# Performance work log

Hardware: AMD Instinct MI355X
Metric: run time of the kernel (lower is better)

## Reference

```python
import jax, jax.numpy as jnp
import numpy as np

D_IN, D_OUT, ORDER, N = 1024, 8192, 3, 2048


def _make_hmap(key, d_in, d_out):
    k1, k2 = jax.random.split(key)
    # h = floor(rand * D_out), row index per input feature
    h = jnp.floor(jax.random.uniform(k1, (d_in,)) * d_out).astype(jnp.int32)
    # w = round(rand) * 2 - 1  -> +/-1 signs
    w = jnp.round(jax.random.uniform(k2, (d_in,))) * 2.0 - 1.0
    # dense [D_out, D_in] with exactly one nonzero per column (faithful to to_dense())
    hm = jnp.zeros((d_out, d_in), dtype=jnp.float32)
    return hm.at[h, jnp.arange(d_in)].set(w.astype(jnp.float32))


def setup_inputs() -> dict:
    key = jax.random.key(0)
    kx, kh = jax.random.split(key)
    x = jax.random.normal(kx, (D_IN, N), dtype=jnp.float32)
    hkeys = jax.random.split(kh, ORDER)
    hmaps = jnp.stack([_make_hmap(hkeys[i], D_IN, D_OUT) for i in range(ORDER)])  # [order, D_out, D_in]
    return {"x": x, "hmaps": hmaps}


def reference(x, hmaps):
    # count[i] = (hmaps[i] @ x).T : [order, N, D_out]
    count = jnp.einsum('odi,in->ond', hmaps, x)
    # torch.rfft(onesided=False) == full complex FFT along last dim
    F = jnp.fft.fft(count, axis=-1)  # complex64, [order, N, D_out]
    # P starts at 1+0j and accumulates complex products over orders
    P = jnp.prod(F, axis=0)  # [N, D_out]
    # torch.irfft(onesided=False) returns real part of inverse FFT
    result = jnp.fft.ifft(P, axis=-1).real.astype(x.dtype)  # [N, D_out]
    return result.T  # [D_out, N]
```

## Files before the change

### kernel.cpp

```cpp
#include <hip/hip_runtime.h>

#define D_IN   1024
#define D_OUTD 8192
#define ORDER  3
#define NCOL   2048

__device__ float2 g_tw[D_OUTD / 2];
__device__ int    g_h[ORDER * D_IN];
__device__ float  g_w[ORDER * D_IN];

__global__ void tw_kernel() {
    int k = blockIdx.x * 256 + threadIdx.x;
    if (k < D_OUTD / 2) {
        double ang = -2.0 * 3.14159265358979323846 * (double)k / (double)D_OUTD;
        g_tw[k] = make_float2((float)cos(ang), (float)sin(ang));
    }
}

__global__ void extract_kernel(const float* __restrict__ hmaps) {
    int idx = blockIdx.x * 256 + threadIdx.x;
    if (idx >= ORDER * D_OUTD * D_IN) return;
    float v = hmaps[idx];
    if (v != 0.0f) {
        int i   = idx % D_IN;
        int rem = idx / D_IN;
        int d   = rem % D_OUTD;
        int o   = rem / D_OUTD;
        g_h[o * D_IN + i] = d;
        g_w[o * D_IN + i] = v;
    }
}

__global__ void xt_kernel(const float* __restrict__ in, float* __restrict__ out) {
    __shared__ float tile[32][33];
    int i0 = blockIdx.x * 32;
    int n0 = blockIdx.y * 32;
    int tx = threadIdx.x;
    int ty = threadIdx.y;
#pragma unroll
    for (int j = 0; j < 32; j += 8)
        tile[ty + j][tx] = in[(i0 + ty + j) * NCOL + n0 + tx];
    __syncthreads();
#pragma unroll
    for (int j = 0; j < 32; j += 8)
        out[(n0 + ty + j) * D_IN + i0 + tx] = tile[tx][ty + j];
}

__device__ __forceinline__ float2 cmul(float2 a, float2 b) {
    return make_float2(a.x * b.x - a.y * b.y, a.x * b.y + a.y * b.x);
}
__device__ __forceinline__ float2 csqr(float2 a) {
    return make_float2(a.x * a.x - a.y * a.y, 2.0f * a.x * a.y);
}
__device__ __forceinline__ float2 c16(int k) {
    constexpr float R[8] = { 1.0f,  0.92387953251128674f,  0.70710678118654757f,  0.38268343236508978f,
                             0.0f, -0.38268343236508978f, -0.70710678118654757f, -0.92387953251128674f };
    constexpr float I[8] = { 0.0f, -0.38268343236508978f, -0.70710678118654757f, -0.92387953251128674f,
                            -1.0f, -0.92387953251128674f, -0.70710678118654757f, -0.38268343236508978f };
    return make_float2(R[k], I[k]);
}

#define FWD_FFT(XR, XI)                                                          \
    {                                                                            \
        float2 ba = wt;                                                          \
        _Pragma("unroll")                                                        \
        for (int m = 3; m >= 0; --m) {                                           \
            const int half = 1 << m;                                             \
            float2 tw[8];                                                        \
            _Pragma("unroll")                                                    \
            for (int lo = 0; lo < half; ++lo) tw[lo] = cmul(ba, c16(lo << (3 - m))); \
            _Pragma("unroll")                                                    \
            for (int p = 0; p < 8; ++p) {                                        \
                const int lo = p & (half - 1);                                   \
                const int hi = p >> m;                                           \
                const int j0 = (hi << (m + 1)) + lo;                             \
                const int j1 = j0 + half;                                        \
                const float2 w = tw[lo];                                         \
                float ar = XR[j0], ai = XI[j0];                                  \
                float br = XR[j1], bi = XI[j1];                                  \
                XR[j0] = ar + br; XI[j0] = ai + bi;                              \
                float dr = ar - br, di = ai - bi;                                \
                XR[j1] = dr * w.x - di * w.y;                                    \
                XI[j1] = dr * w.y + di * w.x;                                    \
            }                                                                    \
            if (m) ba = csqr(ba);                                                \
        }                                                                        \
    }                                                                            \
    _Pragma("unroll")                                                            \
    for (int j = 0; j < 16; ++j) { bre[t + 512 * j] = XR[j]; bim[t + 512 * j] = XI[j]; } \
    __syncthreads();                                                             \
    _Pragma("unroll")                                                            \
    for (int j = 0; j < 16; ++j) { XR[j] = bre[base + 32 * j]; XI[j] = bim[base + 32 * j]; } \
    __syncthreads();                                                             \
    {                                                                            \
        float2 bb = bb16;                                                        \
        _Pragma("unroll")                                                        \
        for (int m = 3; m >= 0; --m) {                                           \
            const int half = 1 << m;                                             \
            float2 tw[8];                                                        \
            _Pragma("unroll")                                                    \
            for (int lo = 0; lo < half; ++lo) tw[lo] = cmul(bb, c16(lo << (3 - m))); \
            _Pragma("unroll")                                                    \
            for (int p = 0; p < 8; ++p) {                                        \
                const int lo = p & (half - 1);                                   \
                const int hi = p >> m;                                           \
                const int j0 = (hi << (m + 1)) + lo;                             \
                const int j1 = j0 + half;                                        \
                const float2 w = tw[lo];                                         \
                float ar = XR[j0], ai = XI[j0];                                  \
                float br = XR[j1], bi = XI[j1];                                  \
                XR[j0] = ar + br; XI[j0] = ai + bi;                              \
                float dr = ar - br, di = ai - bi;                                \
                XR[j1] = dr * w.x - di * w.y;                                    \
                XI[j1] = dr * w.y + di * w.x;                                    \
            }                                                                    \
            if (m) bb = csqr(bb);                                                \
        }                                                                        \
    }                                                                            \
    _Pragma("unroll")                                                            \
    for (int lh = 4; lh >= 0; --lh) {                                            \
        const int st = 1 << lh;                                                  \
        float2 w = tc[lh];                                                       \
        const bool up = (s & st) != 0;                                           \
        const float sg = up ? -1.0f : 1.0f;                                      \
        if (!up) { w.x = 1.0f; w.y = 0.0f; }                                     \
        _Pragma("unroll")                                                        \
        for (int j = 0; j < 16; ++j) {                                           \
            float pr = __shfl_xor(XR[j], st, 64);                                \
            float pi = __shfl_xor(XI[j], st, 64);                                \
            float tr = pr + sg * XR[j];                                          \
            float ti = pi + sg * XI[j];                                          \
            XR[j] = tr * w.x - ti * w.y;                                         \
            XI[j] = tr * w.y + ti * w.x;                                         \
        }                                                                        \
    }

__launch_bounds__(512, 2)
__global__ void sketch_kernel(const float* __restrict__ x, float* __restrict__ outbuf,
                              int staged, int xcoal) {
    __shared__ float bre[D_OUTD];
    __shared__ float bim[D_OUTD];
    const int n0 = 2 * blockIdx.x;
    const int n1 = n0 + 1;
    const int t = threadIdx.x;
    const int s = t & 31;
    const int base = ((t >> 5) << 9) + s;

    float xA0, xA1, xB0, xB1;
    if (xcoal) {
        xA0 = x[n0 * D_IN + t]; xA1 = x[n0 * D_IN + t + 512];
        xB0 = x[n1 * D_IN + t]; xB1 = x[n1 * D_IN + t + 512];
    } else {
        xA0 = x[t * NCOL + n0]; xA1 = x[(t + 512) * NCOL + n0];
        xB0 = x[t * NCOL + n1]; xB1 = x[(t + 512) * NCOL + n1];
    }

    const float2 wt  = g_tw[t];
    const float2 ws  = g_tw[s];
    const float2 w15 = g_tw[s & 15];
    const float2 bb16 = csqr(csqr(csqr(csqr(ws))));
    float2 t4 = w15;
#pragma unroll
    for (int q = 0; q < 8; ++q) t4 = csqr(t4);
    const float sg3 = ((s >> 3) & 1) ? -1.0f : 1.0f;
    const float sg2 = ((s >> 2) & 1) ? -1.0f : 1.0f;
    const float sg1 = ((s >> 1) & 1) ? -1.0f : 1.0f;
    float2 t3 = csqr(t4); t3.x *= sg3; t3.y *= sg3;
    float2 t2 = csqr(t3); t2.x *= sg2; t2.y *= sg2;
    float2 t1 = csqr(t2); t1.x *= sg1; t1.y *= sg1;
    const float2 tc[5] = { make_float2(1.0f, 0.0f), t1, t2, t3, t4 };

    float P0r[16], P0i[16];
    float P1r[16], P1i[16];

    {
        float Ar[16], Ai[16];
#pragma unroll
        for (int j = 0; j < 16; ++j) { bre[t + 512 * j] = 0.0f; bim[t + 512 * j] = 0.0f; }
        __syncthreads();
        {
            const int   h2a = g_h[2 * D_IN + t];
            const float w2a = g_w[2 * D_IN + t];
            const int   h2b = g_h[2 * D_IN + t + 512];
            const float w2b = g_w[2 * D_IN + t + 512];
            atomicAdd(&bre[h2a], w2a * xA0);
            atomicAdd(&bre[h2b], w2b * xA1);
            atomicAdd(&bim[h2a], w2a * xB0);
            atomicAdd(&bim[h2b], w2b * xB1);
        }
        __syncthreads();
#pragma unroll
        for (int j = 0; j < 16; ++j) { Ar[j] = bre[t + 512 * j]; Ai[j] = bim[t + 512 * j]; }
        __syncthreads();

        FWD_FFT(Ar, Ai)

#pragma unroll
        for (int j = 0; j < 16; ++j) { bre[base + 32 * j] = Ar[j]; bim[base + 32 * j] = Ai[j]; }
        __syncthreads();
#pragma unroll
        for (int j = 0; j < 16; ++j) {
            const int q  = base + 32 * j;
            const int sq = q ? (q ^ ((1 << (31 - __clz(q))) - 1)) : 0;
            const float pbr =  bre[sq];
            const float pbi = -bim[sq];
            P0r[j] =  0.5f * (Ar[j] + pbr);
            P0i[j] =  0.5f * (Ai[j] + pbi);
            P1r[j] =  0.5f * (Ai[j] - pbi);
            P1i[j] = -0.5f * (Ar[j] - pbr);
        }
        __syncthreads();
    }

    {
        float Ar[16], Ai[16];
#pragma unroll
        for (int j = 0; j < 16; ++j) { bre[t + 512 * j] = 0.0f; bim[t + 512 * j] = 0.0f; }
        __syncthreads();
        {
            atomicAdd(&bre[g_h[t]],              g_w[t]              * xA0);
            atomicAdd(&bre[g_h[t + 512]],        g_w[t + 512]        * xA1);
            atomicAdd(&bim[g_h[D_IN + t]],       g_w[D_IN + t]       * xA0);
            atomicAdd(&bim[g_h[D_IN + t + 512]], g_w[D_IN + t + 512] * xA1);
        }
        __syncthreads();
#pragma unroll
        for (int j = 0; j < 16; ++j) { Ar[j] = bre[t + 512 * j]; Ai[j] = bim[t + 512 * j]; }
        __syncthreads();

        FWD_FFT(Ar, Ai)

#pragma unroll
        for (int j = 0; j < 16; ++j) { bre[base + 32 * j] = Ar[j]; bim[base + 32 * j] = Ai[j]; }
        __syncthreads();
#pragma unroll
        for (int j = 0; j < 16; ++j) {
            const int q  = base + 32 * j;
            const int sq = q ? (q ^ ((1 << (31 - __clz(q))) - 1)) : 0;
            const float pbr =  bre[sq];
            const float pbi = -bim[sq];
            const float a2r = Ar[j] * Ar[j] - Ai[j] * Ai[j];
            const float a2i = 2.0f * Ar[j] * Ai[j];
            const float b2r = pbr * pbr - pbi * pbi;
            const float b2i = 2.0f * pbr * pbi;
            const float gr =  0.25f * (a2i - b2i);
            const float gi = -0.25f * (a2r - b2r);
            const float fr = P0r[j], fi = P0i[j];
            P0r[j] = gr * fr - gi * fi;
            P0i[j] = gr * fi + gi * fr;
        }
        __syncthreads();
    }

    {
        float Ar[16], Ai[16];
#pragma unroll
        for (int j = 0; j < 16; ++j) { bre[t + 512 * j] = 0.0f; bim[t + 512 * j] = 0.0f; }
        __syncthreads();
        {
            atomicAdd(&bre[g_h[t]],              g_w[t]              * xB0);
            atomicAdd(&bre[g_h[t + 512]],        g_w[t + 512]        * xB1);
            atomicAdd(&bim[g_h[D_IN + t]],       g_w[D_IN + t]       * xB0);
            atomicAdd(&bim[g_h[D_IN + t + 512]], g_w[D_IN + t + 512] * xB1);
        }
        __syncthreads();
#pragma unroll
        for (int j = 0; j < 16; ++j) { Ar[j] = bre[t + 512 * j]; Ai[j] = bim[t + 512 * j]; }
        __syncthreads();

        FWD_FFT(Ar, Ai)

#pragma unroll
        for (int j = 0; j < 16; ++j) { bre[base + 32 * j] = Ar[j]; bim[base + 32 * j] = Ai[j]; }
        __syncthreads();
#pragma unroll
        for (int j = 0; j < 16; ++j) {
            const int q  = base + 32 * j;
            const int sq = q ? (q ^ ((1 << (31 - __clz(q))) - 1)) : 0;
            const float pbr =  bre[sq];
            const float pbi = -bim[sq];
            const float a2r = Ar[j] * Ar[j] - Ai[j] * Ai[j];
            const float a2i = 2.0f * Ar[j] * Ai[j];
            const float b2r = pbr * pbr - pbi * pbi;
            const float b2i = 2.0f * pbr * pbi;
            const float gr =  0.25f * (a2i - b2i);
            const float gi = -0.25f * (a2r - b2r);
            const float fr = P1r[j], fi = P1i[j];
            P1r[j] = gr * fr - gi * fi;
            P1i[j] = gr * fi + gi * fr;
        }
        __syncthreads();
    }

    float Qr[16], Qi[16];
#pragma unroll
    for (int j = 0; j < 16; ++j) {
        Qr[j] = P0r[j] - P1i[j];
        Qi[j] = P0i[j] + P1r[j];
    }

#pragma unroll
    for (int lh = 0; lh <= 4; ++lh) {
        const int st = 1 << lh;
        float2 w = tc[lh];
        w.y = -w.y;
        const bool up = (s & st) != 0;
        const float sg = up ? -1.0f : 1.0f;
        if (!up) { w.x = 1.0f; w.y = 0.0f; }
#pragma unroll
        for (int j = 0; j < 16; ++j) {
            float er = Qr[j] * w.x - Qi[j] * w.y;
            float ei = Qr[j] * w.y + Qi[j] * w.x;
            float pr = __shfl_xor(er, st, 64);
            float pi = __shfl_xor(ei, st, 64);
            Qr[j] = pr + sg * er;
            Qi[j] = pi + sg * ei;
        }
    }

    {
        const float2 bb32 = csqr(bb16), bb64 = csqr(bb32), bb128 = csqr(bb64);
        const float2 bbs[4] = { bb128, bb64, bb32, bb16 };
#pragma unroll
        for (int m = 0; m <= 3; ++m) {
            const int half = 1 << m;
            float2 tw[8];
#pragma unroll
            for (int lo = 0; lo < half; ++lo) tw[lo] = cmul(bbs[m], c16(lo << (3 - m)));
#pragma unroll
            for (int p = 0; p < 8; ++p) {
                const int lo = p & (half - 1);
                const int hi = p >> m;
                const int j0 = (hi << (m + 1)) + lo;
                const int j1 = j0 + half;
                const float2 w = tw[lo];
                float tr = Qr[j1] * w.x + Qi[j1] * w.y;
                float ti = Qi[j1] * w.x - Qr[j1] * w.y;
                Qr[j1] = Qr[j0] - tr; Qi[j1] = Qi[j0] - ti;
                Qr[j0] += tr; Qi[j0] += ti;
            }
        }
    }

#pragma unroll
    for (int j = 0; j < 16; ++j) { bre[base + 32 * j] = Qr[j]; bim[base + 32 * j] = Qi[j]; }
    __syncthreads();
#pragma unroll
    for (int j = 0; j < 16; ++j) { Qr[j] = bre[t + 512 * j]; Qi[j] = bim[t + 512 * j]; }

    {
        const float2 ba2 = csqr(wt), ba4 = csqr(ba2), ba8 = csqr(ba4);
        const float2 bas[4] = { ba8, ba4, ba2, wt };
#pragma unroll
        for (int m = 0; m <= 3; ++m) {
            const int half = 1 << m;
            float2 tw[8];
#pragma unroll
            for (int lo = 0; lo < half; ++lo) tw[lo] = cmul(bas[m], c16(lo << (3 - m)));
#pragma unroll
            for (int p = 0; p < 8; ++p) {
                const int lo = p & (half - 1);
                const int hi = p >> m;
                const int j0 = (hi << (m + 1)) + lo;
                const int j1 = j0 + half;
                const float2 w = tw[lo];
                float tr = Qr[j1] * w.x + Qi[j1] * w.y;
                float ti = Qi[j1] * w.x - Qr[j1] * w.y;
                Qr[j1] = Qr[j0] - tr; Qi[j1] = Qi[j0] - ti;
                Qr[j0] += tr; Qi[j0] += ti;
            }
        }
    }

    const float scale = 1.0f / (float)D_OUTD;
    if (staged) {
#pragma unroll
        for (int j = 0; j < 16; ++j) {
            outbuf[n0 * D_OUTD + t + 512 * j] = Qr[j] * scale;
            outbuf[n1 * D_OUTD + t + 512 * j] = Qi[j] * scale;
        }
    } else {
#pragma unroll
        for (int j = 0; j < 16; ++j) {
            outbuf[(t + 512 * j) * NCOL + n0] = Qr[j] * scale;
            outbuf[(t + 512 * j) * NCOL + n1] = Qi[j] * scale;
        }
    }
}

__global__ void transpose_kernel(const float* __restrict__ in, float* __restrict__ out) {
    __shared__ float tile[32][33];
    int d0 = blockIdx.x * 32;
    int n0 = blockIdx.y * 32;
    int tx = threadIdx.x;
    int ty = threadIdx.y;
#pragma unroll
    for (int j = 0; j < 32; j += 8)
        tile[ty + j][tx] = in[(n0 + ty + j) * D_OUTD + d0 + tx];
    __syncthreads();
#pragma unroll
    for (int j = 0; j < 32; j += 8)
        out[(d0 + ty + j) * NCOL + n0 + tx] = tile[tx][ty + j];
}

extern "C" void kernel_launch(void* const* d_in, const int* in_sizes, int n_in,
                              void* d_out, int out_size, void* d_ws, size_t ws_size,
                              hipStream_t stream) {
    (void)in_sizes; (void)n_in; (void)out_size;
    const float* x     = (const float*)d_in[0];
    const float* hmaps = (const float*)d_in[1];
    float* out = (float*)d_out;

    tw_kernel<<<(D_OUTD / 2 + 255) / 256, 256, 0, stream>>>();
    extract_kernel<<<(ORDER * D_OUTD * D_IN + 255) / 256, 256, 0, stream>>>(hmaps);

    const size_t stage_bytes = (size_t)NCOL * D_OUTD * sizeof(float);
    const size_t xt_bytes    = (size_t)NCOL * D_IN * sizeof(float);

    const float* xs = x;
    int xcoal = 0;
    if (ws_size >= stage_bytes + xt_bytes) {
        float* xT = (float*)((char*)d_ws + stage_bytes);
        xt_kernel<<<dim3(D_IN / 32, NCOL / 32), dim3(32, 8), 0, stream>>>(x, xT);
        xs = xT;
        xcoal = 1;
    }

    if (ws_size >= stage_bytes) {
        float* stag = (float*)d_ws;
        sketch_kernel<<<NCOL / 2, 512, 0, stream>>>(xs, stag, 1, xcoal);
        transpose_kernel<<<dim3(D_OUTD / 32, NCOL / 32), dim3(32, 8), 0, stream>>>(stag, out);
    } else {
        sketch_kernel<<<NCOL / 2, 512, 0, stream>>>(xs, out, 0, xcoal);
    }
}
```

Baseline: 198.6 us.

## Replace warp-shuffle FFT stages with shared-memory passes using swizzled interleaved complex buffer

```diff
diff --git a/kernel.cpp b/kernel.cpp
--- a/kernel.cpp
+++ b/kernel.cpp
@@ -60,15 +60,15 @@
     return make_float2(R[k], I[k]);
 }
 
-#define FWD_FFT(XR, XI)                                                          \
+#define REG_PHASE_FWD(XR, XI, BASE)                                              \
     {                                                                            \
-        float2 ba = wt;                                                          \
+        float2 ba_ = (BASE);                                                     \
         _Pragma("unroll")                                                        \
         for (int m = 3; m >= 0; --m) {                                           \
             const int half = 1 << m;                                             \
             float2 tw[8];                                                        \
             _Pragma("unroll")                                                    \
-            for (int lo = 0; lo < half; ++lo) tw[lo] = cmul(ba, c16(lo << (3 - m))); \
+            for (int lo = 0; lo < half; ++lo) tw[lo] = cmul(ba_, c16(lo << (3 - m))); \
             _Pragma("unroll")                                                    \
             for (int p = 0; p < 8; ++p) {                                        \
                 const int lo = p & (half - 1);                                   \
@@ -83,23 +83,19 @@
                 XR[j1] = dr * w.x - di * w.y;                                    \
                 XI[j1] = dr * w.y + di * w.x;                                    \
             }                                                                    \
-            if (m) ba = csqr(ba);                                                \
+            if (m) ba_ = csqr(ba_);                                              \
         }                                                                        \
-    }                                                                            \
-    _Pragma("unroll")                                                            \
-    for (int j = 0; j < 16; ++j) { bre[t + 512 * j] = XR[j]; bim[t + 512 * j] = XI[j]; } \
-    __syncthreads();                                                             \
-    _Pragma("unroll")                                                            \
-    for (int j = 0; j < 16; ++j) { XR[j] = bre[base + 32 * j]; XI[j] = bim[base + 32 * j]; } \
-    __syncthreads();                                                             \
+    }
+
+#define REG_PHASE_INV(XR, XI, B8, B4, B2, B1)                                    \
     {                                                                            \
-        float2 bb = bb16;                                                        \
+        const float2 bas_[4] = { (B8), (B4), (B2), (B1) };                       \
         _Pragma("unroll")                                                        \
-        for (int m = 3; m >= 0; --m) {                                           \
+        for (int m = 0; m <= 3; ++m) {                                           \
             const int half = 1 << m;                                             \
             float2 tw[8];                                                        \
             _Pragma("unroll")                                                    \
-            for (int lo = 0; lo < half; ++lo) tw[lo] = cmul(bb, c16(lo << (3 - m))); \
+            for (int lo = 0; lo < half; ++lo) tw[lo] = cmul(bas_[m], c16(lo << (3 - m))); \
             _Pragma("unroll")                                                    \
             for (int p = 0; p < 8; ++p) {                                        \
                 const int lo = p & (half - 1);                                   \
@@ -107,44 +103,51 @@
                 const int j0 = (hi << (m + 1)) + lo;                             \
                 const int j1 = j0 + half;                                        \
                 const float2 w = tw[lo];                                         \
-                float ar = XR[j0], ai = XI[j0];                                  \
-                float br = XR[j1], bi = XI[j1];                                  \
-                XR[j0] = ar + br; XI[j0] = ai + bi;                              \
-                float dr = ar - br, di = ai - bi;                                \
-                XR[j1] = dr * w.x - di * w.y;                                    \
-                XI[j1] = dr * w.y + di * w.x;                                    \
+                float tr = XR[j1] * w.x + XI[j1] * w.y;                          \
+                float ti = XI[j1] * w.x - XR[j1] * w.y;                          \
+                XR[j1] = XR[j0] - tr; XI[j1] = XI[j0] - ti;                      \
+                XR[j0] += tr; XI[j0] += ti;                                      \
             }                                                                    \
-            if (m) bb = csqr(bb);                                                \
         }                                                                        \
-    }                                                                            \
-    _Pragma("unroll")                                                            \
-    for (int lh = 4; lh >= 0; --lh) {                                            \
-        const int st = 1 << lh;                                                  \
-        float2 w = tc[lh];                                                       \
-        const bool up = (s & st) != 0;                                           \
-        const float sg = up ? -1.0f : 1.0f;                                      \
-        if (!up) { w.x = 1.0f; w.y = 0.0f; }                                     \
-        _Pragma("unroll")                                                        \
-        for (int j = 0; j < 16; ++j) {                                           \
-            float pr = __shfl_xor(XR[j], st, 64);                                \
-            float pi = __shfl_xor(XI[j], st, 64);                                \
-            float tr = pr + sg * XR[j];                                          \
-            float ti = pi + sg * XI[j];                                          \
-            XR[j] = tr * w.x - ti * w.y;                                         \
-            XI[j] = tr * w.y + ti * w.x;                                         \
-        }                                                                        \
-    }
+    }
+
+#define FWD_CORE(XR, XI)                                                         \
+    _Pragma("unroll")                                                            \
+    for (int j = 0; j < 16; ++j) { float2 v_ = buf[tA + 512 * j]; XR[j] = v_.x; XI[j] = v_.y; } \
+    REG_PHASE_FWD(XR, XI, wt)                                                    \
+    _Pragma("unroll")                                                            \
+    for (int j = 0; j < 16; ++j) buf[tA + 512 * j] = make_float2(XR[j], XI[j]);  \
+    __syncthreads();                                                             \
+    _Pragma("unroll")                                                            \
+    for (int j = 0; j < 16; ++j) { float2 v_ = buf[bB + 32 * j + (s ^ (j << 1))]; XR[j] = v_.x; XI[j] = v_.y; } \
+    REG_PHASE_FWD(XR, XI, bb16)                                                  \
+    _Pragma("unroll")                                                            \
+    for (int j = 0; j < 16; ++j) buf[bB + 32 * j + (s ^ (j << 1))] = make_float2(XR[j], XI[j]); \
+    __syncthreads();                                                             \
+    _Pragma("unroll")                                                            \
+    for (int j = 0; j < 16; ++j) { float2 v_ = buf[pc + 2 * (j ^ kc)]; XR[j] = v_.x; XI[j] = v_.y; } \
+    REG_PHASE_FWD(XR, XI, bc)                                                    \
+    _Pragma("unroll")                                                            \
+    for (int j = 0; j < 16; ++j) buf[pc + 2 * (j ^ kc)] = make_float2(XR[j], XI[j]); \
+    __syncthreads();
 
 __launch_bounds__(512, 2)
 __global__ void sketch_kernel(const float* __restrict__ x, float* __restrict__ outbuf,
                               int staged, int xcoal) {
-    __shared__ float bre[D_OUTD];
-    __shared__ float bim[D_OUTD];
+    __shared__ __align__(16) float2 buf[D_OUTD];
     const int n0 = 2 * blockIdx.x;
     const int n1 = n0 + 1;
     const int t = threadIdx.x;
+    const int e = t & 1;
     const int s = t & 31;
-    const int base = ((t >> 5) << 9) + s;
+    const int kA = ((t >> 5) & 15) << 1;
+    const int tA = t ^ kA;
+    const int bB = 512 * (t >> 5);
+    const int kc = (t >> 1) & 15;
+    const int pp = 32 * (t >> 1);
+    const int pc = pp + e;
+    const int qc0 = pp + e;
+    const float sgE = e ? -1.0f : 1.0f;
 
     float xA0, xA1, xB0, xB1;
     if (xcoal) {
@@ -155,59 +158,52 @@
         xB0 = x[t * NCOL + n1]; xB1 = x[(t + 512) * NCOL + n1];
     }
 
-    const float2 wt  = g_tw[t];
-    const float2 ws  = g_tw[s];
-    const float2 w15 = g_tw[s & 15];
+    const float2 wt   = g_tw[t];
+    const float2 ws   = g_tw[s];
     const float2 bb16 = csqr(csqr(csqr(csqr(ws))));
-    float2 t4 = w15;
-#pragma unroll
-    for (int q = 0; q < 8; ++q) t4 = csqr(t4);
-    const float sg3 = ((s >> 3) & 1) ? -1.0f : 1.0f;
-    const float sg2 = ((s >> 2) & 1) ? -1.0f : 1.0f;
-    const float sg1 = ((s >> 1) & 1) ? -1.0f : 1.0f;
-    float2 t3 = csqr(t4); t3.x *= sg3; t3.y *= sg3;
-    float2 t2 = csqr(t3); t2.x *= sg2; t2.y *= sg2;
-    float2 t1 = csqr(t2); t1.x *= sg1; t1.y *= sg1;
-    const float2 tc[5] = { make_float2(1.0f, 0.0f), t1, t2, t3, t4 };
-
-    float P0r[16], P0i[16];
-    float P1r[16], P1i[16];
+    const float2 bc   = e ? make_float2(0.98078528040323044f, -0.19509032201612825f)
+                          : make_float2(1.0f, 0.0f);
+
+    float P0r[16], P0i[16], P1r[16], P1i[16];
 
     {
         float Ar[16], Ai[16];
 #pragma unroll
-        for (int j = 0; j < 16; ++j) { bre[t + 512 * j] = 0.0f; bim[t + 512 * j] = 0.0f; }
+        for (int j = 0; j < 16; ++j) buf[tA + 512 * j] = make_float2(0.0f, 0.0f);
         __syncthreads();
         {
-            const int   h2a = g_h[2 * D_IN + t];
-            const float w2a = g_w[2 * D_IN + t];
-            const int   h2b = g_h[2 * D_IN + t + 512];
-            const float w2b = g_w[2 * D_IN + t + 512];
-            atomicAdd(&bre[h2a], w2a * xA0);
-            atomicAdd(&bre[h2b], w2b * xA1);
-            atomicAdd(&bim[h2a], w2a * xB0);
-            atomicAdd(&bim[h2b], w2b * xB1);
-        }
-        __syncthreads();
-#pragma unroll
-        for (int j = 0; j < 16; ++j) { Ar[j] = bre[t + 512 * j]; Ai[j] = bim[t + 512 * j]; }
-        __syncthreads();
-
-        FWD_FFT(Ar, Ai)
-
-#pragma unroll
-        for (int j = 0; j < 16; ++j) { bre[base + 32 * j] = Ar[j]; bim[base + 32 * j] = Ai[j]; }
-        __syncthreads();
+            const int   h0 = g_h[2 * D_IN + t];
+            const float w0 = g_w[2 * D_IN + t];
+            const int   h1 = g_h[2 * D_IN + t + 512];
+            const float w1 = g_w[2 * D_IN + t + 512];
+            const int   p0 = h0 ^ (((h0 >> 5) & 15) << 1);
+            const int   p1 = h1 ^ (((h1 >> 5) & 15) << 1);
+            atomicAdd(&buf[p0].x, w0 * xA0);
+            atomicAdd(&buf[p0].y, w0 * xB0);
+            atomicAdd(&buf[p1].x, w1 * xA1);
+            atomicAdd(&buf[p1].y, w1 * xB1);
+        }
+        __syncthreads();
+
+        FWD_CORE(Ar, Ai)
+
 #pragma unroll
         for (int j = 0; j < 16; ++j) {
-            const int q  = base + 32 * j;
-            const int sq = q ? (q ^ ((1 << (31 - __clz(q))) - 1)) : 0;
-            const float pbr =  bre[sq];
-            const float pbi = -bim[sq];
-            P0r[j] =  0.5f * (Ar[j] + pbr);
-            P0i[j] =  0.5f * (Ai[j] + pbi);
-            P1r[j] =  0.5f * (Ai[j] - pbi);
-            P1i[j] = -0.5f * (Ar[j] - pbr);
+            const int q = qc0 + 2 * j;
+            const float4 ov = *reinterpret_cast<const float4*>(&buf[pp + 2 * (j ^ kc)]);
+            const int L   = 31 - __clz(q | 1);
+            const int pb  = (q ^ ((1 << L) - 1)) & ~1;
+            const int pph = pb ^ (((pb >> 5) & 15) << 1);
+            const float4 pv = *reinterpret_cast<const float4*>(&buf[pph]);
+            const float sgP = (q < 2) ? sgE : -sgE;
+            const float ar  = ov.x + sgE * ov.z;
+            const float ai  = ov.y + sgE * ov.w;
+            const float pbr =  (pv.x + sgP * pv.z);
+            const float pbi = -(pv.y + sgP * pv.w);
+            P0r[j] =  0.5f * (ar + pbr);
+            P0i[j] =  0.5f * (ai + pbi);
+            P1r[j] =  0.5f * (ai - pbi);
+            P1i[j] = -0.5f * (ar - pbr);
         }
         __syncthreads();
     }
@@ -215,32 +211,41 @@
     {
         float Ar[16], Ai[16];
 #pragma unroll
-        for (int j = 0; j < 16; ++j) { bre[t + 512 * j] = 0.0f; bim[t + 512 * j] = 0.0f; }
+        for (int j = 0; j < 16; ++j) buf[tA + 512 * j] = make_float2(0.0f, 0.0f);
         __syncthreads();
         {
-            atomicAdd(&bre[g_h[t]],              g_w[t]              * xA0);
-            atomicAdd(&bre[g_h[t + 512]],        g_w[t + 512]        * xA1);
-            atomicAdd(&bim[g_h[D_IN + t]],       g_w[D_IN + t]       * xA0);
-            atomicAdd(&bim[g_h[D_IN + t + 512]], g_w[D_IN + t + 512] * xA1);
-        }
-        __syncthreads();
-#pragma unroll
-        for (int j = 0; j < 16; ++j) { Ar[j] = bre[t + 512 * j]; Ai[j] = bim[t + 512 * j]; }
-        __syncthreads();
-
-        FWD_FFT(Ar, Ai)
-
-#pragma unroll
-        for (int j = 0; j < 16; ++j) { bre[base + 32 * j] = Ar[j]; bim[base + 32 * j] = Ai[j]; }
-        __syncthreads();
+            const int   h0 = g_h[t];            const float w0 = g_w[t];
+            const int   h1 = g_h[t + 512];      const float w1 = g_w[t + 512];
+            const int   h2 = g_h[D_IN + t];     const float w2 = g_w[D_IN + t];
+            const int   h3 = g_h[D_IN + t + 512]; const float w3 = g_w[D_IN + t + 512];
+            const int   p0 = h0 ^ (((h0 >> 5) & 15) << 1);
+            const int   p1 = h1 ^ (((h1 >> 5) & 15) << 1);
+            const int   p2 = h2 ^ (((h2 >> 5) & 15) << 1);
+            const int   p3 = h3 ^ (((h3 >> 5) & 15) << 1);
+            atomicAdd(&buf[p0].x, w0 * xA0);
+            atomicAdd(&buf[p1].x, w1 * xA1);
+            atomicAdd(&buf[p2].y, w2 * xA0);
+            atomicAdd(&buf[p3].y, w3 * xA1);
+        }
+        __syncthreads();
+
+        FWD_CORE(Ar, Ai)
+
 #pragma unroll
         for (int j = 0; j < 16; ++j) {
-            const int q  = base + 32 * j;
-            const int sq = q ? (q ^ ((1 << (31 - __clz(q))) - 1)) : 0;
-            const float pbr =  bre[sq];
-            const float pbi = -bim[sq];
-            const float a2r = Ar[j] * Ar[j] - Ai[j] * Ai[j];
-            const float a2i = 2.0f * Ar[j] * Ai[j];
+            const int q = qc0 + 2 * j;
+            const float4 ov = *reinterpret_cast<const float4*>(&buf[pp + 2 * (j ^ kc)]);
+            const int L   = 31 - __clz(q | 1);
+            const int pb  = (q ^ ((1 << L) - 1)) & ~1;
+            const int pph = pb ^ (((pb >> 5) & 15) << 1);
+            const float4 pv = *reinterpret_cast<const float4*>(&buf[pph]);
+            const float sgP = (q < 2) ? sgE : -sgE;
+            const float ar  = ov.x + sgE * ov.z;
+            const float ai  = ov.y + sgE * ov.w;
+            const float pbr =  (pv.x + sgP * pv.z);
+            const float pbi = -(pv.y + sgP * pv.w);
+            const float a2r = ar * ar - ai * ai;
+            const float a2i = 2.0f * ar * ai;
             const float b2r = pbr * pbr - pbi * pbi;
             const float b2i = 2.0f * pbr * pbi;
             const float gr =  0.25f * (a2i - b2i);
@@ -255,32 +260,41 @@
     {
         float Ar[16], Ai[16];
 #pragma unroll
-        for (int j = 0; j < 16; ++j) { bre[t + 512 * j] = 0.0f; bim[t + 512 * j] = 0.0f; }
+        for (int j = 0; j < 16; ++j) buf[tA + 512 * j] = make_float2(0.0f, 0.0f);
         __syncthreads();
         {
-            atomicAdd(&bre[g_h[t]],              g_w[t]              * xB0);
-            atomicAdd(&bre[g_h[t + 512]],        g_w[t + 512]        * xB1);
-            atomicAdd(&bim[g_h[D_IN + t]],       g_w[D_IN + t]       * xB0);
-            atomicAdd(&bim[g_h[D_IN + t + 512]], g_w[D_IN + t + 512] * xB1);
-        }
-        __syncthreads();
-#pragma unroll
-        for (int j = 0; j < 16; ++j) { Ar[j] = bre[t + 512 * j]; Ai[j] = bim[t + 512 * j]; }
-        __syncthreads();
-
-        FWD_FFT(Ar, Ai)
-
-#pragma unroll
-        for (int j = 0; j < 16; ++j) { bre[base + 32 * j] = Ar[j]; bim[base + 32 * j] = Ai[j]; }
-        __syncthreads();
+            const int   h0 = g_h[t];            const float w0 = g_w[t];
+            const int   h1 = g_h[t + 512];      const float w1 = g_w[t + 512];
+            const int   h2 = g_h[D_IN + t];     const float w2 = g_w[D_IN + t];
+            const int   h3 = g_h[D_IN + t + 512]; const float w3 = g_w[D_IN + t + 512];
+            const int   p0 = h0 ^ (((h0 >> 5) & 15) << 1);
+            const int   p1 = h1 ^ (((h1 >> 5) & 15) << 1);
+            const int   p2 = h2 ^ (((h2 >> 5) & 15) << 1);
+            const int   p3 = h3 ^ (((h3 >> 5) & 15) << 1);
+            atomicAdd(&buf[p0].x, w0 * xB0);
+            atomicAdd(&buf[p1].x, w1 * xB1);
+            atomicAdd(&buf[p2].y, w2 * xB0);
+            atomicAdd(&buf[p3].y, w3 * xB1);
+        }
+        __syncthreads();
+
+        FWD_CORE(Ar, Ai)
+
 #pragma unroll
         for (int j = 0; j < 16; ++j) {
-            const int q  = base + 32 * j;
-            const int sq = q ? (q ^ ((1 << (31 - __clz(q))) - 1)) : 0;
-            const float pbr =  bre[sq];
-            const float pbi = -bim[sq];
-            const float a2r = Ar[j] * Ar[j] - Ai[j] * Ai[j];
-            const float a2i = 2.0f * Ar[j] * Ai[j];
+            const int q = qc0 + 2 * j;
+            const float4 ov = *reinterpret_cast<const float4*>(&buf[pp + 2 * (j ^ kc)]);
+            const int L   = 31 - __clz(q | 1);
+            const int pb  = (q ^ ((1 << L) - 1)) & ~1;
+            const int pph = pb ^ (((pb >> 5) & 15) << 1);
+            const float4 pv = *reinterpret_cast<const float4*>(&buf[pph]);
+            const float sgP = (q < 2) ? sgE : -sgE;
+            const float ar  = ov.x + sgE * ov.z;
+            const float ai  = ov.y + sgE * ov.w;
+            const float pbr =  (pv.x + sgP * pv.z);
+            const float pbi = -(pv.y + sgP * pv.w);
+            const float a2r = ar * ar - ai * ai;
+            const float a2i = 2.0f * ar * ai;
             const float b2r = pbr * pbr - pbi * pbi;
             const float b2i = 2.0f * pbr * pbi;
             const float gr =  0.25f * (a2i - b2i);
@@ -300,76 +314,38 @@
     }
 
 #pragma unroll
-    for (int lh = 0; lh <= 4; ++lh) {
-        const int st = 1 << lh;
-        float2 w = tc[lh];
-        w.y = -w.y;
-        const bool up = (s & st) != 0;
-        const float sg = up ? -1.0f : 1.0f;
-        if (!up) { w.x = 1.0f; w.y = 0.0f; }
-#pragma unroll
-        for (int j = 0; j < 16; ++j) {
-            float er = Qr[j] * w.x - Qi[j] * w.y;
-            float ei = Qr[j] * w.y + Qi[j] * w.x;
-            float pr = __shfl_xor(er, st, 64);
-            float pi = __shfl_xor(ei, st, 64);
-            Qr[j] = pr + sg * er;
-            Qi[j] = pi + sg * ei;
-        }
-    }
+    for (int j = 0; j < 16; ++j) {
+        const float orr = __shfl_xor(Qr[j], 1, 64);
+        const float oii = __shfl_xor(Qi[j], 1, 64);
+        Qr[j] = orr + sgE * Qr[j];
+        Qi[j] = oii + sgE * Qi[j];
+    }
+
+    {
+        const float2 bc2 = csqr(bc), bc4 = csqr(bc2), bc8 = csqr(bc4);
+        REG_PHASE_INV(Qr, Qi, bc8, bc4, bc2, bc)
+    }
+
+#pragma unroll
+    for (int j = 0; j < 16; ++j) buf[pc + 2 * (j ^ kc)] = make_float2(Qr[j], Qi[j]);
+    __syncthreads();
+#pragma unroll
+    for (int j = 0; j < 16; ++j) { float2 v_ = buf[bB + 32 * j + (s ^ (j << 1))]; Qr[j] = v_.x; Qi[j] = v_.y; }
 
     {
         const float2 bb32 = csqr(bb16), bb64 = csqr(bb32), bb128 = csqr(bb64);
-        const float2 bbs[4] = { bb128, bb64, bb32, bb16 };
-#pragma unroll
-        for (int m = 0; m <= 3; ++m) {
-            const int half = 1 << m;
-            float2 tw[8];
-#pragma unroll
-            for (int lo = 0; lo < half; ++lo) tw[lo] = cmul(bbs[m], c16(lo << (3 - m)));
-#pragma unroll
-            for (int p = 0; p < 8; ++p) {
-                const int lo = p & (half - 1);
-                const int hi = p >> m;
-                const int j0 = (hi << (m + 1)) + lo;
-                const int j1 = j0 + half;
-                const float2 w = tw[lo];
-                float tr = Qr[j1] * w.x + Qi[j1] * w.y;
-                float ti = Qi[j1] * w.x - Qr[j1] * w.y;
-                Qr[j1] = Qr[j0] - tr; Qi[j1] = Qi[j0] - ti;
-                Qr[j0] += tr; Qi[j0] += ti;
-            }
-        }
-    }
-
-#pragma unroll
-    for (int j = 0; j < 16; ++j) { bre[base + 32 * j] = Qr[j]; bim[base + 32 * j] = Qi[j]; }
+        REG_PHASE_INV(Qr, Qi, bb128, bb64, bb32, bb16)
+    }
+
+#pragma unroll
+    for (int j = 0; j < 16; ++j) buf[bB + 32 * j + (s ^ (j << 1))] = make_float2(Qr[j], Qi[j]);
     __syncthreads();
 #pragma unroll
-    for (int j = 0; j < 16; ++j) { Qr[j] = bre[t + 512 * j]; Qi[j] = bim[t + 512 * j]; }
-
-    {
-        const float2 ba2 = csqr(wt), ba4 = csqr(ba2), ba8 = csqr(ba4);
-        const float2 bas[4] = { ba8, ba4, ba2, wt };
-#pragma unroll
-        for (int m = 0; m <= 3; ++m) {
-            const int half = 1 << m;
-            float2 tw[8];
-#pragma unroll
-            for (int lo = 0; lo < half; ++lo) tw[lo] = cmul(bas[m], c16(lo << (3 - m)));
-#pragma unroll
-            for (int p = 0; p < 8; ++p) {
-                const int lo = p & (half - 1);
-                const int hi = p >> m;
-                const int j0 = (hi << (m + 1)) + lo;
-                const int j1 = j0 + half;
-                const float2 w = tw[lo];
-                float tr = Qr[j1] * w.x + Qi[j1] * w.y;
-                float ti = Qi[j1] * w.x - Qr[j1] * w.y;
-                Qr[j1] = Qr[j0] - tr; Qi[j1] = Qi[j0] - ti;
-                Qr[j0] += tr; Qi[j0] += ti;
-            }
-        }
+    for (int j = 0; j < 16; ++j) { float2 v_ = buf[tA + 512 * j]; Qr[j] = v_.x; Qi[j] = v_.y; }
+
+    {
+        const float2 wa2 = csqr(wt), wa4 = csqr(wa2), wa8 = csqr(wa4);
+        REG_PHASE_INV(Qr, Qi, wa8, wa4, wa2, wt)
     }
 
     const float scale = 1.0f / (float)D_OUTD;
```

After: 442.4 us. 123% more time.
